# Kernel tuning notes

Hardware: AMD Instinct MI355X
Metric: run time of the kernel (lower is better)

Reference implementation:

```python
import jax, jax.numpy as jnp
import numpy as np

HIDDEN = 2048
HEADS = 16
HEAD_DIM = HIDDEN // HEADS  # 128
SCALE = 1.0 / float(np.sqrt(HEAD_DIM))
B, S = 2, 2048


def setup_inputs() -> dict:
    key = jax.random.key(0)
    ks = jax.random.split(key, 5)
    return {
        "x": jax.random.normal(ks[0], (B, S, HIDDEN), dtype=jnp.float32),
        "q_w": jax.random.normal(ks[1], (HIDDEN, HIDDEN), dtype=jnp.float32) * (HIDDEN ** -0.5),
        "k_w": jax.random.normal(ks[2], (HEAD_DIM, HIDDEN), dtype=jnp.float32) * (HIDDEN ** -0.5),
        "v_w": jax.random.normal(ks[3], (HEAD_DIM, HIDDEN), dtype=jnp.float32) * (HIDDEN ** -0.5),
        "o_w": jax.random.normal(ks[4], (HIDDEN, HIDDEN), dtype=jnp.float32) * (HIDDEN ** -0.5),
    }


def reference(x, q_w, k_w, v_w, o_w):
    b, s, _ = x.shape
    # torch F.linear: x @ W^T with W [out, in]
    q = (x @ q_w.T).reshape(b, s, HEADS, HEAD_DIM).transpose(0, 2, 1, 3)  # [B,H,S,D]
    k = x @ k_w.T  # [B,S,D] single shared KV head
    v = x @ v_w.T  # [B,S,D]
    # scores: [B,H,S,S] -- explicit O(S^2) materialization as in the source
    scores = jnp.einsum('bhqd,bkd->bhqk', q, k) * SCALE
    # softmax in float32 then cast back (matches dtype=torch.float32 then type_as)
    attn = jax.nn.softmax(scores.astype(jnp.float32), axis=-1).astype(q.dtype)
    out = jnp.einsum('bhqk,bkd->bhqd', attn, v)  # [B,H,S,D]
    out = out.transpose(0, 2, 1, 3).reshape(b, s, HIDDEN)
    return out @ o_w.T
```

## Files before the change

### kernel.cpp

```cpp
#include <hip/hip_runtime.h>
#include <stdint.h>

#define HID 2048
#define DHEAD 128
#define SEQL 2048
#define C2 0.1275187981510609f
#define MOFF 8.0f

typedef __attribute__((ext_vector_type(4))) float f32x4;
typedef __attribute__((ext_vector_type(16))) float f32x16;
typedef __attribute__((ext_vector_type(8))) short s16x8;

__device__ __forceinline__ unsigned short bf16_rne(float f) {
  union { float f; unsigned u; } v; v.f = f;
  return (unsigned short)((v.u + 0x7FFFu + ((v.u >> 16) & 1u)) >> 16);
}

__device__ __forceinline__ void gload_lds16(const void* g, void* l) {
  __builtin_amdgcn_global_load_lds(
      (__attribute__((address_space(1))) unsigned int*)(void*)g,
      (__attribute__((address_space(3))) unsigned int*)l, 16, 0, 0);
}

__device__ __forceinline__ void cvt8(const float* __restrict__ in,
                                     unsigned short* __restrict__ out, int k) {
  const f32x4* p = (const f32x4*)in;
  f32x4 a = p[2 * k], b = p[2 * k + 1];
  union { s16x8 v; unsigned short s[8]; } o;
  o.s[0] = bf16_rne(a[0]); o.s[1] = bf16_rne(a[1]);
  o.s[2] = bf16_rne(a[2]); o.s[3] = bf16_rne(a[3]);
  o.s[4] = bf16_rne(b[0]); o.s[5] = bf16_rne(b[1]);
  o.s[6] = bf16_rne(b[2]); o.s[7] = bf16_rne(b[3]);
  ((s16x8*)out)[k] = o.v;
}

__global__ __launch_bounds__(256) void cvt_bf16_k(const float* __restrict__ in,
                                                  unsigned short* __restrict__ out,
                                                  int n8) {
  int i = blockIdx.x * 256 + threadIdx.x;
  if (i >= n8) return;
  cvt8(in, out, i);
}

__global__ __launch_bounds__(256) void cvt4_k(
    const float* __restrict__ s0, unsigned short* __restrict__ d0, int n0,
    const float* __restrict__ s1, unsigned short* __restrict__ d1, int n1,
    const float* __restrict__ s2, unsigned short* __restrict__ d2, int n2,
    const float* __restrict__ s3, unsigned short* __restrict__ d3, int n3) {
  int i = blockIdx.x * 256 + threadIdx.x;
  if (i < n0) { cvt8(s0, d0, i); return; }
  i -= n0;
  if (i < n1) { cvt8(s1, d1, i); return; }
  i -= n1;
  if (i < n2) { cvt8(s2, d2, i); return; }
  i -= n2;
  if (i < n3) { cvt8(s3, d3, i); return; }
}

__global__ __launch_bounds__(256) void cvt5_k(
    const float* __restrict__ s0, unsigned short* __restrict__ d0, int n0,
    const float* __restrict__ s1, unsigned short* __restrict__ d1, int n1,
    const float* __restrict__ s2, unsigned short* __restrict__ d2, int n2,
    const float* __restrict__ s3, unsigned short* __restrict__ d3, int n3,
    const float* __restrict__ s4, unsigned short* __restrict__ d4, int n4) {
  int i = blockIdx.x * 256 + threadIdx.x;
  if (i < n0) { cvt8(s0, d0, i); return; }
  i -= n0;
  if (i < n1) { cvt8(s1, d1, i); return; }
  i -= n1;
  if (i < n2) { cvt8(s2, d2, i); return; }
  i -= n2;
  if (i < n3) { cvt8(s3, d3, i); return; }
  i -= n3;
  if (i < n4) { cvt8(s4, d4, i); return; }
}

__device__ __forceinline__ void stage_tile512(const unsigned short* __restrict__ src,
                                              int ld, char* smem, int t) {
#pragma unroll
  for (int i = 0; i < 2; ++i) {
    int c = i * 512 + t;
    int row = c >> 3;
    int slot = c & 7;
    gload_lds16(src + row * ld + ((slot ^ (row & 7)) << 3),
                smem + (i * 512 + (t >> 6) * 64) * 16);
  }
}

template <int MODE>
__global__ __launch_bounds__(512, 4) void gemm_bt(
    const unsigned short* __restrict__ A, const unsigned short* __restrict__ Bw,
    void* __restrict__ Cout, int M, int N, int K,
    unsigned short* __restrict__ Kb, unsigned short* __restrict__ Vt) {
  __shared__ char As[2][16384];
  __shared__ char Bs[2][16384];
  int t = threadIdx.x;
  int lane = t & 63, w = t >> 6;
  int wm = w >> 2, wn = w & 3;
  int l15 = lane & 15, l4 = lane >> 4;

  int gdx = gridDim.x;
  int nwg = gdx * gridDim.y;
  int bid = blockIdx.y * gdx + blockIdx.x;
  int q8 = nwg >> 3;
  int swz = (bid & 7) * q8 + (bid >> 3);
  int tm = (swz / gdx) * 128, tn = (swz % gdx) * 128;

  f32x4 acc[4][2] = {};

  stage_tile512(A + tm * K, K, As[0], t);
  stage_tile512(Bw + tn * K, K, Bs[0], t);
  stage_tile512(A + tm * K + 64, K, As[1], t);
  stage_tile512(Bw + tn * K + 64, K, Bs[1], t);

  int nk = K >> 6;
  for (int ki = 0; ki < nk; ++ki) {
    int cur = ki & 1;
    if (ki < nk - 1) asm volatile("s_waitcnt vmcnt(4)" ::: "memory");
    else             asm volatile("s_waitcnt vmcnt(0)" ::: "memory");
    __builtin_amdgcn_sched_barrier(0);
    __builtin_amdgcn_s_barrier();

    const char* as = As[cur];
    const char* bs = Bs[cur];
    s16x8 af[4][2], bfr[2][2];
#pragma unroll
    for (int m = 0; m < 4; ++m)
#pragma unroll
      for (int kk = 0; kk < 2; ++kk) {
        int row = wm * 64 + m * 16 + l15;
        af[m][kk] = *(const s16x8*)(as + row * 128 + (((kk * 4 + l4) ^ (row & 7)) << 4));
      }
#pragma unroll
    for (int n = 0; n < 2; ++n)
#pragma unroll
      for (int kk = 0; kk < 2; ++kk) {
        int row = wn * 32 + n * 16 + l15;
        bfr[n][kk] = *(const s16x8*)(bs + row * 128 + (((kk * 4 + l4) ^ (row & 7)) << 4));
      }
    asm volatile("s_waitcnt lgkmcnt(0)" ::: "memory");
    __builtin_amdgcn_sched_barrier(0);
    __builtin_amdgcn_s_barrier();
    if (ki + 2 < nk) {
      stage_tile512(A + tm * K + (ki + 2) * 64, K, As[cur], t);
      stage_tile512(Bw + tn * K + (ki + 2) * 64, K, Bs[cur], t);
    }
    __builtin_amdgcn_s_setprio(1);
#pragma unroll
    for (int m = 0; m < 4; ++m)
#pragma unroll
      for (int n = 0; n < 2; ++n)
#pragma unroll
        for (int kk = 0; kk < 2; ++kk)
          acc[m][n] = __builtin_amdgcn_mfma_f32_16x16x32_bf16(af[m][kk], bfr[n][kk],
                                                              acc[m][n], 0, 0, 0);
    __builtin_amdgcn_s_setprio(0);
  }

#pragma unroll
  for (int m = 0; m < 4; ++m)
#pragma unroll
    for (int n = 0; n < 2; ++n) {
      int col = tn + wn * 32 + n * 16 + l15;
#pragma unroll
      for (int j = 0; j < 4; ++j) {
        int row = tm + wm * 64 + m * 16 + l4 * 4 + j;
        float v = acc[m][n][j];
        if (MODE == 1) {
          ((float*)Cout)[row * N + col] = v;
        } else {
          if (col < 2048) {
            ((unsigned short*)Cout)[row * 2048 + col] = bf16_rne(v);
          } else if (col < 2176) {
            Kb[row * 128 + (col - 2048)] = bf16_rne(v);
          } else {
            int d = col - 2176, bb = row >> 11, s = row & 2047;
            Vt[((bb * 128 + d) << 11) + s] = bf16_rne(v);
          }
        }
      }
    }
}

__global__ __launch_bounds__(256, 2) void attn_k(
    const unsigned short* __restrict__ Q, const unsigned short* __restrict__ Kb,
    const unsigned short* __restrict__ Vt, unsigned short* __restrict__ AO) {
  __shared__ char Ks[2][16384];
  __shared__ char Vs[2][16384];
  int t = threadIdx.x;
  int lane = t & 63, w = t >> 6;
  int l31 = lane & 31, lh = lane >> 5;
  int qt = blockIdx.x, bh = blockIdx.y;
  int b = bh >> 4, h = bh & 15;
  int qg = b * SEQL + qt * 128 + w * 32;

  s16x8 qf[8];
#pragma unroll
  for (int kc = 0; kc < 8; ++kc)
    qf[kc] = *(const s16x8*)(Q + (qg + l31) * HID + h * DHEAD + kc * 16 + lh * 8);

  union { s16x8 v; unsigned short s[8]; } one_;
#pragma unroll
  for (int i = 0; i < 8; ++i) one_.s[i] = 0x3F80;
  const s16x8 onesb = one_.v;

  f32x16 oacc[4] = {};
  f32x16 dacc = {};

#pragma unroll
  for (int i = 0; i < 4; ++i) {
    int c = i * 256 + t, row = c >> 4, slot = c & 15;
    gload_lds16(Kb + (b * SEQL + row) * DHEAD + ((slot ^ (row & 7)) << 3),
                Ks[0] + (i * 256 + w * 64) * 16);
  }
#pragma unroll
  for (int i = 0; i < 4; ++i) {
    int c = i * 256 + t, row = c >> 3, slot = c & 7;
    gload_lds16(Vt + (b * DHEAD + row) * SEQL + ((slot ^ (row & 7)) << 3),
                Vs[0] + (i * 256 + w * 64) * 16);
  }
  asm volatile("s_waitcnt vmcnt(0)" ::: "memory");
  __builtin_amdgcn_s_barrier();

  for (int kv = 0; kv < SEQL; kv += 64) {
    int cur = (kv >> 6) & 1;
    if (kv + 64 < SEQL) {
#pragma unroll
      for (int i = 0; i < 4; ++i) {
        int c = i * 256 + t, row = c >> 4, slot = c & 15;
        gload_lds16(Kb + (b * SEQL + kv + 64 + row) * DHEAD + ((slot ^ (row & 7)) << 3),
                    Ks[cur ^ 1] + (i * 256 + w * 64) * 16);
      }
#pragma unroll
      for (int i = 0; i < 4; ++i) {
        int c = i * 256 + t, row = c >> 3, slot = c & 7;
        gload_lds16(Vt + (b * DHEAD + row) * SEQL + kv + 64 + ((slot ^ (row & 7)) << 3),
                    Vs[cur ^ 1] + (i * 256 + w * 64) * 16);
      }
    }

    const char* ks = Ks[cur];
    const char* vs = Vs[cur];

    f32x16 s0 = {}, s1 = {};
    __builtin_amdgcn_s_setprio(1);
#pragma unroll
    for (int kc = 0; kc < 8; ++kc) {
      int slot = kc * 2 + lh;
      int r0 = l31, r1 = 32 + l31;
      s16x8 kf0 = *(const s16x8*)(ks + r0 * 256 + ((slot ^ (r0 & 7)) << 4));
      s16x8 kf1 = *(const s16x8*)(ks + r1 * 256 + ((slot ^ (r1 & 7)) << 4));
      s0 = __builtin_amdgcn_mfma_f32_32x32x16_bf16(kf0, qf[kc], s0, 0, 0, 0);
      s1 = __builtin_amdgcn_mfma_f32_32x32x16_bf16(kf1, qf[kc], s1, 0, 0, 0);
    }
    __builtin_amdgcn_s_setprio(0);

    s16x8 paf[4];
#pragma unroll
    for (int g = 0; g < 2; ++g)
#pragma unroll
      for (int half = 0; half < 2; ++half) {
        unsigned u[4];
#pragma unroll
        for (int i = 0; i < 4; ++i) {
          float pe = __builtin_amdgcn_exp2f(__builtin_fmaf(
              (g ? s1 : s0)[half * 8 + 2 * i], C2, -MOFF));
          float po = __builtin_amdgcn_exp2f(__builtin_fmaf(
              (g ? s1 : s0)[half * 8 + 2 * i + 1], C2, -MOFF));
          u[i] = (__builtin_bit_cast(unsigned, po) & 0xFFFF0000u) |
                 (__builtin_bit_cast(unsigned, pe) >> 16);
        }
        asm("v_permlane32_swap_b32 %0, %1" : "+v"(u[0]), "+v"(u[2]));
        asm("v_permlane32_swap_b32 %0, %1" : "+v"(u[1]), "+v"(u[3]));
        union { unsigned uu[4]; s16x8 v; } pk;
        pk.uu[0] = u[0]; pk.uu[1] = u[1]; pk.uu[2] = u[2]; pk.uu[3] = u[3];
        paf[g * 2 + half] = pk.v;
      }

    __builtin_amdgcn_s_setprio(1);
#pragma unroll
    for (int kstep = 0; kstep < 4; ++kstep) {
#pragma unroll
      for (int dg = 0; dg < 4; ++dg) {
        int vrow = dg * 32 + l31;
        int slot = kstep * 2 + lh;
        s16x8 vf = *(const s16x8*)(vs + vrow * 128 + ((slot ^ (vrow & 7)) << 4));
        oacc[dg] = __builtin_amdgcn_mfma_f32_32x32x16_bf16(paf[kstep], vf, oacc[dg], 0, 0, 0);
      }
      dacc = __builtin_amdgcn_mfma_f32_32x32x16_bf16(paf[kstep], onesb, dacc, 0, 0, 0);
    }
    __builtin_amdgcn_s_setprio(0);

    asm volatile("s_waitcnt vmcnt(0) lgkmcnt(0)" ::: "memory");
    __builtin_amdgcn_sched_barrier(0);
    __builtin_amdgcn_s_barrier();
  }

  float inv[16];
#pragma unroll
  for (int r = 0; r < 16; ++r) inv[r] = 1.f / dacc[r];
#pragma unroll
  for (int dg = 0; dg < 4; ++dg)
#pragma unroll
    for (int r = 0; r < 16; ++r) {
      int qi = (r & 3) + 8 * (r >> 2) + 4 * lh;
      AO[(qg + qi) * HID + h * DHEAD + dg * 32 + l31] = bf16_rne(oacc[dg][r] * inv[r]);
    }
}

extern "C" void kernel_launch(void* const* d_in, const int* in_sizes, int n_in,
                              void* d_out, int out_size, void* d_ws, size_t ws_size,
                              hipStream_t stream) {
  const float* x  = (const float*)d_in[0];
  const float* qw = (const float*)d_in[1];
  const float* kw = (const float*)d_in[2];
  const float* vw = (const float*)d_in[3];
  const float* ow = (const float*)d_in[4];

  char* ws = (char*)d_ws;
  unsigned short* xb   = (unsigned short*)(ws);
  unsigned short* qwb  = (unsigned short*)(ws + 16777216);
  unsigned short* kvwb = (unsigned short*)(ws + 25165824);
  unsigned short* Qb   = (unsigned short*)(ws + 26214400);
  unsigned short* Kbuf = (unsigned short*)(ws + 42991616);
  unsigned short* Vtb  = (unsigned short*)(ws + 44040192);
  unsigned short* AOb  = xb;

  bool big = ws_size >= 54525953ull;
  unsigned short* owb = big ? (unsigned short*)(ws + 46137344) : qwb;

  if (big) {
    cvt5_k<<<8448, 256, 0, stream>>>(x, xb, 1048576, qw, qwb, 524288,
                                     kw, kvwb, 32768, vw, kvwb + 262144, 32768,
                                     ow, owb, 524288);
  } else {
    cvt4_k<<<6400, 256, 0, stream>>>(x, xb, 1048576, qw, qwb, 524288,
                                     kw, kvwb, 32768, vw, kvwb + 262144, 32768);
  }

  gemm_bt<0><<<dim3(18, 32), 512, 0, stream>>>(xb, qwb, Qb, 4096, 2304, 2048, Kbuf, Vtb);
  if (!big) {
    cvt_bf16_k<<<2048, 256, 0, stream>>>(ow, owb, 524288);
  }
  attn_k<<<dim3(16, 32), 256, 0, stream>>>(Qb, Kbuf, Vtb, AOb);
  gemm_bt<1><<<dim3(16, 32), 512, 0, stream>>>(AOb, owb, d_out, 4096, 2048, 2048,
                                               nullptr, nullptr);
}
```

Before: 194.8 us.

## Split attention KV sequence across two wave groups with LDS reduction

The attention block grows from 256 to 512 threads, and the two halves of waves each cover half of the KV sequence (1024 keys). This is possible because the softmax uses a fixed max offset, so partial sums can simply be added. Each half keeps one K and one V LDS buffer instead of double-buffering. K and V loads are staggered inside the iteration with extra barriers, so the next K load overlaps the softmax and the V load comes after the PV MFMAs. At the end the upper half writes its partial O and denominator to LDS, and the lower half adds them, normalizes and stores. This is meant to double the waves per CU to hide latency, at the cost of more barriers, no double buffering, and a reduction epilogue.

```diff
diff --git a/kernel.cpp b/kernel.cpp
--- a/kernel.cpp
+++ b/kernel.cpp
@@ -182,17 +182,22 @@
     }
 }
 
-__global__ __launch_bounds__(256, 2) void attn_k(
+__global__ __launch_bounds__(512, 4) void attn_k(
     const unsigned short* __restrict__ Q, const unsigned short* __restrict__ Kb,
     const unsigned short* __restrict__ Vt, unsigned short* __restrict__ AO) {
   __shared__ char Ks[2][16384];
   __shared__ char Vs[2][16384];
   int t = threadIdx.x;
   int lane = t & 63, w = t >> 6;
+  int qq = w & 3, hf = w >> 2;
+  int tl = t & 255;
+  int wq = qq;
   int l31 = lane & 31, lh = lane >> 5;
   int qt = blockIdx.x, bh = blockIdx.y;
   int b = bh >> 4, h = bh & 15;
-  int qg = b * SEQL + qt * 128 + w * 32;
+  int qg = b * SEQL + qt * 128 + qq * 32;
+  const unsigned short* Kh = Kb + (b * SEQL + hf * 1024) * DHEAD;
+  const unsigned short* Vh = Vt + b * DHEAD * SEQL + hf * 1024;
 
   s16x8 qf[8];
 #pragma unroll
@@ -209,38 +214,22 @@
 
 #pragma unroll
   for (int i = 0; i < 4; ++i) {
-    int c = i * 256 + t, row = c >> 4, slot = c & 15;
-    gload_lds16(Kb + (b * SEQL + row) * DHEAD + ((slot ^ (row & 7)) << 3),
-                Ks[0] + (i * 256 + w * 64) * 16);
+    int c = i * 256 + tl, row = c >> 4, slot = c & 15;
+    gload_lds16(Kh + row * DHEAD + ((slot ^ (row & 7)) << 3),
+                Ks[hf] + (i * 256 + wq * 64) * 16);
   }
 #pragma unroll
   for (int i = 0; i < 4; ++i) {
-    int c = i * 256 + t, row = c >> 3, slot = c & 7;
-    gload_lds16(Vt + (b * DHEAD + row) * SEQL + ((slot ^ (row & 7)) << 3),
-                Vs[0] + (i * 256 + w * 64) * 16);
+    int c = i * 256 + tl, row = c >> 3, slot = c & 7;
+    gload_lds16(Vh + row * SEQL + ((slot ^ (row & 7)) << 3),
+                Vs[hf] + (i * 256 + wq * 64) * 16);
   }
   asm volatile("s_waitcnt vmcnt(0)" ::: "memory");
   __builtin_amdgcn_s_barrier();
 
-  for (int kv = 0; kv < SEQL; kv += 64) {
-    int cur = (kv >> 6) & 1;
-    if (kv + 64 < SEQL) {
-#pragma unroll
-      for (int i = 0; i < 4; ++i) {
-        int c = i * 256 + t, row = c >> 4, slot = c & 15;
-        gload_lds16(Kb + (b * SEQL + kv + 64 + row) * DHEAD + ((slot ^ (row & 7)) << 3),
-                    Ks[cur ^ 1] + (i * 256 + w * 64) * 16);
-      }
-#pragma unroll
-      for (int i = 0; i < 4; ++i) {
-        int c = i * 256 + t, row = c >> 3, slot = c & 7;
-        gload_lds16(Vt + (b * DHEAD + row) * SEQL + kv + 64 + ((slot ^ (row & 7)) << 3),
-                    Vs[cur ^ 1] + (i * 256 + w * 64) * 16);
-      }
-    }
-
-    const char* ks = Ks[cur];
-    const char* vs = Vs[cur];
+  for (int it = 0; it < 16; ++it) {
+    const char* ks = Ks[hf];
+    const char* vs = Vs[hf];
 
     f32x16 s0 = {}, s1 = {};
     __builtin_amdgcn_s_setprio(1);
@@ -254,6 +243,19 @@
       s1 = __builtin_amdgcn_mfma_f32_32x32x16_bf16(kf1, qf[kc], s1, 0, 0, 0);
     }
     __builtin_amdgcn_s_setprio(0);
+
+    asm volatile("s_waitcnt lgkmcnt(0)" ::: "memory");
+    __builtin_amdgcn_sched_barrier(0);
+    __builtin_amdgcn_s_barrier();
+
+    if (it < 15) {
+#pragma unroll
+      for (int i = 0; i < 4; ++i) {
+        int c = i * 256 + tl, row = c >> 4, slot = c & 15;
+        gload_lds16(Kh + ((it + 1) * 64 + row) * DHEAD + ((slot ^ (row & 7)) << 3),
+                    Ks[hf] + (i * 256 + wq * 64) * 16);
+      }
+    }
 
     s16x8 paf[4];
 #pragma unroll
@@ -277,6 +279,11 @@
         paf[g * 2 + half] = pk.v;
       }
 
+    if (it < 15) asm volatile("s_waitcnt vmcnt(4)" ::: "memory");
+    else         asm volatile("s_waitcnt vmcnt(0)" ::: "memory");
+    __builtin_amdgcn_sched_barrier(0);
+    __builtin_amdgcn_s_barrier();
+
     __builtin_amdgcn_s_setprio(1);
 #pragma unroll
     for (int kstep = 0; kstep < 4; ++kstep) {
@@ -294,18 +301,61 @@
     asm volatile("s_waitcnt vmcnt(0) lgkmcnt(0)" ::: "memory");
     __builtin_amdgcn_sched_barrier(0);
     __builtin_amdgcn_s_barrier();
+
+    if (it < 15) {
+#pragma unroll
+      for (int i = 0; i < 4; ++i) {
+        int c = i * 256 + tl, row = c >> 3, slot = c & 7;
+        gload_lds16(Vh + row * SEQL + (it + 1) * 64 + ((slot ^ (row & 7)) << 3),
+                    Vs[hf] + (i * 256 + wq * 64) * 16);
+      }
+    }
   }
 
   float inv[16];
-#pragma unroll
-  for (int r = 0; r < 16; ++r) inv[r] = 1.f / dacc[r];
-#pragma unroll
-  for (int dg = 0; dg < 4; ++dg)
-#pragma unroll
-    for (int r = 0; r < 16; ++r) {
-      int qi = (r & 3) + 8 * (r >> 2) + 4 * lh;
-      AO[(qg + qi) * HID + h * DHEAD + dg * 32 + l31] = bf16_rne(oacc[dg][r] * inv[r]);
-    }
+  {
+    float* r0 = ((qq < 2) ? (float*)Ks[0] : (float*)Vs[0]) + (qq & 1) * 3136 + lane * 49;
+    if (hf) {
+#pragma unroll
+      for (int r = 0; r < 16; ++r) r0[r] = oacc[0][r];
+#pragma unroll
+      for (int r = 0; r < 16; ++r) r0[16 + r] = oacc[1][r];
+#pragma unroll
+      for (int r = 0; r < 16; ++r) r0[32 + r] = dacc[r];
+    }
+    __syncthreads();
+    if (!hf) {
+#pragma unroll
+      for (int r = 0; r < 16; ++r) inv[r] = 1.f / (dacc[r] + r0[32 + r]);
+#pragma unroll
+      for (int dg = 0; dg < 2; ++dg)
+#pragma unroll
+        for (int r = 0; r < 16; ++r) {
+          int qi = (r & 3) + 8 * (r >> 2) + 4 * lh;
+          AO[(qg + qi) * HID + h * DHEAD + dg * 32 + l31] =
+              bf16_rne((oacc[dg][r] + r0[dg * 16 + r]) * inv[r]);
+        }
+    }
+    __syncthreads();
+    float* r1 = ((qq < 2) ? (float*)Ks[0] : (float*)Vs[0]) + (qq & 1) * 2112 + lane * 33;
+    if (hf) {
+#pragma unroll
+      for (int r = 0; r < 16; ++r) r1[r] = oacc[2][r];
+#pragma unroll
+      for (int r = 0; r < 16; ++r) r1[16 + r] = oacc[3][r];
+    }
+    __syncthreads();
+    if (!hf) {
+#pragma unroll
+      for (int dg = 2; dg < 4; ++dg)
+#pragma unroll
+        for (int r = 0; r < 16; ++r) {
+          int qi = (r & 3) + 8 * (r >> 2) + 4 * lh;
+          AO[(qg + qi) * HID + h * DHEAD + dg * 32 + l31] =
+              bf16_rne((oacc[dg][r] + r1[(dg - 2) * 16 + r]) * inv[r]);
+        }
+    }
+  }
 }
 
 extern "C" void kernel_launch(void* const* d_in, const int* in_sizes, int n_in,
@@ -342,7 +392,7 @@
   if (!big) {
     cvt_bf16_k<<<2048, 256, 0, stream>>>(ow, owb, 524288);
   }
-  attn_k<<<dim3(16, 32), 256, 0, stream>>>(Qb, Kbuf, Vtb, AOb);
+  attn_k<<<dim3(16, 32), 512, 0, stream>>>(Qb, Kbuf, Vtb, AOb);
   gemm_bt<1><<<dim3(16, 32), 512, 0, stream>>>(AOb, owb, d_out, 4096, 2048, 2048,
                                                nullptr, nullptr);
 }
```

Result: slower. 289.7 us (+48.8%).
